# Kernel tuning notes

Hardware: AMD Instinct MI355X
Metric: run time of the kernel (lower is better)

The kernel has to match this reference:

```python
import jax, jax.numpy as jnp
import numpy as np

B, N, F, K = 512, 128, 128, 4


def setup_inputs() -> dict:
    key = jax.random.key(0)
    ks = jax.random.split(key, 12)
    # xavier-normal-ish scales
    s_rw = float(np.sqrt(2.0 / (F + F)))
    s_sw = float(np.sqrt(2.0 / (F + F)))
    inp = {
        "H": jax.random.normal(ks[0], (B, N, F), dtype=jnp.float32),
        "E": jax.random.uniform(ks[1], (B, N, N, K), dtype=jnp.float32),
        "RW1": jax.random.normal(ks[2], (F, F, K), dtype=jnp.float32) * s_rw,
        "SW1": jax.random.normal(ks[3], (F, F), dtype=jnp.float32) * s_sw,
        "RW2": jax.random.normal(ks[4], (F, F, K), dtype=jnp.float32) * s_rw,
        "SW2": jax.random.normal(ks[5], (F, F), dtype=jnp.float32) * s_sw,
        "RW3": jax.random.normal(ks[6], (F, F, K), dtype=jnp.float32) * s_rw,
        "SW3": jax.random.normal(ks[7], (F, F), dtype=jnp.float32) * s_sw,
        "W1": jax.random.normal(ks[8], (F, 20), dtype=jnp.float32) * float(np.sqrt(1.0 / F)),
        "b1": jnp.zeros((20,), dtype=jnp.float32),
        "W2": jax.random.normal(ks[9], (20, 1), dtype=jnp.float32) * float(np.sqrt(1.0 / 20)),
        "b2": jnp.zeros((1,), dtype=jnp.float32),
    }
    return inp


def _rgcn_conv(H, E, D, RW, SW):
    # einsum('bi,bijk,bjm,mnk->bin') done in two GEMM-shaped steps
    M = jnp.einsum('bijk,bjm->bimk', E, H)          # [B,N,F,K]
    msg = jnp.einsum('bimk,mnk->bin', M, RW)        # [B,N,F]
    return jax.nn.sigmoid(msg * D[:, :, None] + jnp.einsum('bij,jl->bil', H, SW))


def reference(H, E, RW1, SW1, RW2, SW2, RW3, SW3, W1, b1, W2, b2):
    # degree norm with self-loops: (E + eye)[b,i,:,:].sum() = E.sum((2,3)) + K
    k = jnp.asarray(E.shape[-1], dtype=E.dtype)
    D = 1.0 / (E.sum(axis=(2, 3)) + k)              # [B,N]
    H = _rgcn_conv(H, E, D, RW1, SW1)
    H = _rgcn_conv(H, E, D, RW2, SW2)
    H = _rgcn_conv(H, E, D, RW3, SW3)
    h = jnp.maximum(H @ W1 + b1, 0.1 * (H @ W1 + b1))  # LeakyReLU(0.1)
    score = jnp.mean(jax.nn.sigmoid(h @ W2 + b2))
    return score
```

## Files before the change

kernel.cpp:

```cpp
#include <hip/hip_runtime.h>
#include <math.h>

#define BB 512
#define NN 128
#define FF 128
#define KK 4
#define GS_PITCH 132

typedef __attribute__((ext_vector_type(8))) short bf16x8;
typedef __attribute__((ext_vector_type(4))) float f32x4;

__device__ inline unsigned short f2bf(float x) {
  union { float f; unsigned int u; } v; v.f = x;
  unsigned int r = v.u + 0x7fff + ((v.u >> 16) & 1);
  return (unsigned short)(r >> 16);
}
__device__ inline float bf2f(unsigned short h) {
  union { unsigned int u; float f; } v; v.u = ((unsigned int)h) << 16; return v.f;
}

__device__ inline void g2l16(const unsigned short* gptr, unsigned short* lptr) {
  __builtin_amdgcn_global_load_lds(
      (const __attribute__((address_space(1))) unsigned int*)gptr,
      (__attribute__((address_space(3))) unsigned int*)lptr, 16, 0, 0);
}

__global__ __launch_bounds__(256) void k_prep(
    const float* __restrict__ E, const float* __restrict__ H,
    const float* __restrict__ RW1, const float* __restrict__ SW1,
    const float* __restrict__ RW2, const float* __restrict__ SW2,
    const float* __restrict__ RW3, const float* __restrict__ SW3,
    unsigned short* __restrict__ Eb, unsigned short* __restrict__ Ha,
    unsigned short* __restrict__ W2L, float* __restrict__ Dv,
    float* __restrict__ Sum, int* __restrict__ Cnt)
{
  const int bid = blockIdx.x;
  if (bid < 16384) {
    int wave = threadIdx.x >> 6;
    int lane = threadIdx.x & 63;
    int row  = bid * 4 + wave;
    const float* p = E + (size_t)row * 512 + lane * 8;
    f32x4 a = *(const f32x4*)p;
    f32x4 b = *(const f32x4*)(p + 4);
    float s = a[0] + a[1] + a[2] + a[3] + b[0] + b[1] + b[2] + b[3];
    #pragma unroll
    for (int off = 32; off > 0; off >>= 1) s += __shfl_down(s, off, 64);
    if (lane == 0) Dv[row] = 1.0f / (s + 4.0f);
    union { unsigned short h[8]; f32x4 v; } u;
    u.h[0] = f2bf(a[0]); u.h[1] = f2bf(a[1]); u.h[2] = f2bf(a[2]); u.h[3] = f2bf(a[3]);
    u.h[4] = f2bf(b[0]); u.h[5] = f2bf(b[1]); u.h[6] = f2bf(b[2]); u.h[7] = f2bf(b[3]);
    *(f32x4*)(Eb + (size_t)row * 512 + lane * 8) = u.v;
  } else if (bid < 20480) {
    size_t i = ((size_t)(bid - 16384) * 256 + threadIdx.x) * 8;
    f32x4 a = *(const f32x4*)(H + i);
    f32x4 b = *(const f32x4*)(H + i + 4);
    union { unsigned short h[8]; f32x4 v; } u;
    u.h[0] = f2bf(a[0]); u.h[1] = f2bf(a[1]); u.h[2] = f2bf(a[2]); u.h[3] = f2bf(a[3]);
    u.h[4] = f2bf(b[0]); u.h[5] = f2bf(b[1]); u.h[6] = f2bf(b[2]); u.h[7] = f2bf(b[3]);
    *(f32x4*)(Ha + i) = u.v;
  } else {
    int t2  = bid - 20480;
    int tab = t2 / 320;
    int idx = (t2 - tab * 320) * 256 + threadIdx.x;
    int m = idx & 127;
    int c = idx >> 7;
    const float* RW = (tab == 0) ? RW1 : (tab == 1) ? RW2 : RW3;
    const float* SW = (tab == 0) ? SW1 : (tab == 1) ? SW2 : SW3;
    float v = (c < 512) ? RW[m * 512 + c] : SW[m * 128 + (c - 512)];
    W2L[(size_t)tab * 81920 + idx] = f2bf(v);
    if (t2 == 0 && threadIdx.x == 0) { *Sum = 0.0f; *Cnt = 0; }
  }
}

template<int DOMLP>
__global__ __launch_bounds__(512, 2) void k_layer(
    const unsigned short* __restrict__ Eb,
    const unsigned short* __restrict__ Hin,
    const unsigned short* __restrict__ W2L,
    const float* __restrict__ Dv,
    unsigned short* __restrict__ Hout,
    const float* __restrict__ W1, const float* __restrict__ b1,
    const float* __restrict__ W2w, const float* __restrict__ b2,
    float* __restrict__ Sum, int* __restrict__ Cnt, float* __restrict__ out)
{
  __shared__ unsigned short Gs[128 * GS_PITCH];
  __shared__ unsigned short Es[128 * 128];

  const int b = blockIdx.x;
  const unsigned short* E_b = Eb  + (size_t)b * 65536;
  const unsigned short* H_b = Hin + (size_t)b * 16384;

  const int tid = threadIdx.x;
  const int w = tid >> 6, l = tid & 63;
  const int wr = w >> 1, wc = w & 1;
  const int lq = l >> 4, lm = l & 15;

  f32x4 macc[2][4] = {};

  for (int s = 0; s < 4; ++s) {
    if (s) __syncthreads();

    bf16x8 fa0[4], fb0[2];
    #pragma unroll
    for (int f = 0; f < 4; ++f)
      fa0[f] = *(const bf16x8*)(W2L + (w * 64 + f * 16 + lm) * 128 + lq * 8);
    #pragma unroll
    for (int g = 0; g < 2; ++g)
      fb0[g] = *(const bf16x8*)(H_b + (s * 32 + g * 16 + lm) * 128 + lq * 8);

    #pragma unroll
    for (int r = 0; r < 4; ++r) {
      int R   = r * 32 + w * 4 + (l >> 4);
      int cbg = (l & 15) ^ (R & 15);
      g2l16(E_b + R * 512 + s * 128 + cbg * 8,
            Es + (r * 32 + w * 4) * 128);
    }

    f32x4 gacc[4][2] = {};
    #pragma unroll
    for (int f = 0; f < 4; ++f)
      #pragma unroll
      for (int g = 0; g < 2; ++g)
        gacc[f][g] = __builtin_amdgcn_mfma_f32_16x16x32_bf16(fa0[f], fb0[g], gacc[f][g], 0, 0, 0);
    #pragma unroll
    for (int k0 = 32; k0 < 128; k0 += 32) {
      bf16x8 fa[4], fb[2];
      #pragma unroll
      for (int f = 0; f < 4; ++f)
        fa[f] = *(const bf16x8*)(W2L + (w * 64 + f * 16 + lm) * 128 + k0 + lq * 8);
      #pragma unroll
      for (int g = 0; g < 2; ++g)
        fb[g] = *(const bf16x8*)(H_b + (s * 32 + g * 16 + lm) * 128 + k0 + lq * 8);
      #pragma unroll
      for (int f = 0; f < 4; ++f)
        #pragma unroll
        for (int g = 0; g < 2; ++g)
          gacc[f][g] = __builtin_amdgcn_mfma_f32_16x16x32_bf16(fa[f], fb[g], gacc[f][g], 0, 0, 0);
    }
    #pragma unroll
    for (int f = 0; f < 4; ++f) {
      int n = w * 16 + f * 4 + lq;
      #pragma unroll
      for (int g = 0; g < 2; ++g) {
        int jl = g * 16 + lm;
        union { unsigned short h4[4]; uint2 v; } u;
        u.h4[0] = f2bf(gacc[f][g][0]); u.h4[1] = f2bf(gacc[f][g][1]);
        u.h4[2] = f2bf(gacc[f][g][2]); u.h4[3] = f2bf(gacc[f][g][3]);
        *(uint2*)(&Gs[n * GS_PITCH + jl * 4]) = u.v;
      }
    }
    __syncthreads();

    #pragma unroll
    for (int kt = 0; kt < 4; ++kt) {
      bf16x8 ea[2], fb[4];
      #pragma unroll
      for (int f = 0; f < 2; ++f) {
        int i  = wr * 32 + f * 16 + lm;
        int cb = (kt * 4 + lq) ^ lm;
        ea[f] = *(const bf16x8*)(Es + i * 128 + cb * 8);
      }
      #pragma unroll
      for (int g = 0; g < 4; ++g)
        fb[g] = *(const bf16x8*)(&Gs[(wc * 64 + g * 16 + lm) * GS_PITCH + kt * 32 + lq * 8]);
      #pragma unroll
      for (int f = 0; f < 2; ++f)
        #pragma unroll
        for (int g = 0; g < 4; ++g)
          macc[f][g] = __builtin_amdgcn_mfma_f32_16x16x32_bf16(ea[f], fb[g], macc[f][g], 0, 0, 0);
    }
  }

  f32x4 sacc[2][4] = {};
  #pragma unroll
  for (int k0 = 0; k0 < 128; k0 += 32) {
    bf16x8 fa[2], fb[4];
    #pragma unroll
    for (int f = 0; f < 2; ++f)
      fa[f] = *(const bf16x8*)(H_b + (wr * 32 + f * 16 + lm) * 128 + k0 + lq * 8);
    #pragma unroll
    for (int g = 0; g < 4; ++g)
      fb[g] = *(const bf16x8*)(W2L + (512 + wc * 64 + g * 16 + lm) * 128 + k0 + lq * 8);
    #pragma unroll
    for (int f = 0; f < 2; ++f)
      #pragma unroll
      for (int g = 0; g < 4; ++g)
        sacc[f][g] = __builtin_amdgcn_mfma_f32_16x16x32_bf16(fa[f], fb[g], sacc[f][g], 0, 0, 0);
  }

  const float* dvb = Dv + b * 128;
  __syncthreads();
  #pragma unroll
  for (int f = 0; f < 2; ++f) {
    int i0 = wr * 32 + f * 16 + lq * 4;
    f32x4 d = *(const f32x4*)(dvb + i0);
    #pragma unroll
    for (int g = 0; g < 4; ++g) {
      int n = wc * 64 + g * 16 + lm;
      #pragma unroll
      for (int r = 0; r < 4; ++r) {
        float v = fmaf(macc[f][g][r], d[r], sacc[f][g][r]);
        Es[(i0 + r) * 128 + n] = f2bf(1.0f / (1.0f + __expf(-v)));
      }
    }
  }
  __syncthreads();
  unsigned short* O_b = Hout + (size_t)b * 16384;
  {
    int off = tid * 32;
    f32x4 v0 = *(const f32x4*)(Es + off);
    f32x4 v1 = *(const f32x4*)(Es + off + 8);
    f32x4 v2 = *(const f32x4*)(Es + off + 16);
    f32x4 v3 = *(const f32x4*)(Es + off + 24);
    *(f32x4*)(O_b + off)      = v0;
    *(f32x4*)(O_b + off + 8)  = v1;
    *(f32x4*)(O_b + off + 16) = v2;
    *(f32x4*)(O_b + off + 24) = v3;
  }

  if (DOMLP) {
    __syncthreads();
    float* W1s = (float*)Gs;
    float* b1s = W1s + 2560;
    float* W2s = b1s + 32;
    float* red = W2s + 32;
    for (int i = tid; i < 2560; i += 512) W1s[i] = W1[i];
    if (tid < 20) { b1s[tid] = b1[tid]; W2s[tid] = W2w[tid]; }
    __syncthreads();

    float sv = 0.0f;
    if (tid < 128) {
      const unsigned short* hr = O_b + (size_t)tid * 128;
      float h[20];
      #pragma unroll
      for (int j = 0; j < 20; ++j) h[j] = b1s[j];
      for (int m8 = 0; m8 < 128; m8 += 8) {
        f32x4 pk = *(const f32x4*)(hr + m8);
        const unsigned short* us = (const unsigned short*)&pk;
        #pragma unroll
        for (int e = 0; e < 8; ++e) {
          float x = bf2f(us[e]);
          #pragma unroll
          for (int j = 0; j < 20; ++j) h[j] = fmaf(x, W1s[(m8 + e) * 20 + j], h[j]);
        }
      }
      float v = b2[0];
      #pragma unroll
      for (int j = 0; j < 20; ++j) {
        float t = h[j];
        t = fmaxf(t, 0.1f * t);
        v = fmaf(t, W2s[j], v);
      }
      sv = 1.0f / (1.0f + __expf(-v));
    }

    red[tid] = sv;
    __syncthreads();
    #pragma unroll
    for (int off = 256; off > 0; off >>= 1) {
      if (tid < off) red[tid] += red[tid + off];
      __syncthreads();
    }
    if (tid == 0) {
      atomicAdd(Sum, red[0]);
      __threadfence();
      int c = atomicAdd(Cnt, 1);
      if (c == BB - 1) {
        float tot = atomicAdd(Sum, 0.0f);
        out[0] = tot * (1.0f / 65536.0f);
      }
    }
  }
}

extern "C" void kernel_launch(void* const* d_in, const int* in_sizes, int n_in,
                              void* d_out, int out_size, void* d_ws, size_t ws_size,
                              hipStream_t stream) {
  (void)in_sizes; (void)n_in; (void)out_size; (void)ws_size;
  const float* H   = (const float*)d_in[0];
  const float* E   = (const float*)d_in[1];
  const float* RW1 = (const float*)d_in[2];
  const float* SW1 = (const float*)d_in[3];
  const float* RW2 = (const float*)d_in[4];
  const float* SW2 = (const float*)d_in[5];
  const float* RW3 = (const float*)d_in[6];
  const float* SW3 = (const float*)d_in[7];
  const float* W1  = (const float*)d_in[8];
  const float* b1  = (const float*)d_in[9];
  const float* W2  = (const float*)d_in[10];
  const float* b2  = (const float*)d_in[11];
  float* out = (float*)d_out;

  char* w = (char*)d_ws;
  float*          wsD   = (float*)w;           w += (size_t)65536 * 4;
  unsigned short* wsEb  = (unsigned short*)w;  w += (size_t)33554432 * 2;
  unsigned short* wsHa  = (unsigned short*)w;  w += (size_t)8388608 * 2;
  unsigned short* wsHb  = (unsigned short*)w;  w += (size_t)8388608 * 2;
  unsigned short* wsHc  = (unsigned short*)w;  w += (size_t)8388608 * 2;
  unsigned short* wsHd  = (unsigned short*)w;  w += (size_t)8388608 * 2;
  unsigned short* wsW2  = (unsigned short*)w;  w += (size_t)3 * 81920 * 2;
  float*          wsSum = (float*)w;           w += 64;
  int*            wsCnt = (int*)w;             w += 64;

  k_prep<<<21440, 256, 0, stream>>>(E, H, RW1, SW1, RW2, SW2, RW3, SW3,
                                    wsEb, wsHa, wsW2, wsD, wsSum, wsCnt);

  k_layer<0><<<BB, 512, 0, stream>>>(wsEb, wsHa, wsW2,          wsD, wsHb,
                                     W1, b1, W2, b2, wsSum, wsCnt, out);
  k_layer<0><<<BB, 512, 0, stream>>>(wsEb, wsHb, wsW2 + 81920,  wsD, wsHc,
                                     W1, b1, W2, b2, wsSum, wsCnt, out);
  k_layer<1><<<BB, 512, 0, stream>>>(wsEb, wsHc, wsW2 + 163840, wsD, wsHd,
                                     W1, b1, W2, b2, wsSum, wsCnt, out);
}
```

Before: 428.0 us.

## Split MLP tail into separate kernel and use raw barriers in layer loop

Moves the final MLP and mean reduction out of the third layer kernel into a dedicated k_mlp kernel that uses one thread per node row across 256 blocks. This stops the third layer kernel from running a mostly idle tail where only 128 of 512 threads work. Inside the layer loop, __syncthreads is replaced with a raw s_barrier, and the barrier before the MFMA phase waits only on LDS counters (lgkmcnt), not on vmcnt. A sched_barrier is added after the async global-to-LDS E loads so the E-tile copy can overlap the first GEMM. The risk is correctness: Es is filled by global_load_lds, which may count against vmcnt, so waiting only on lgkmcnt could let the MFMA phase read Es before the data lands.

```diff
diff --git a/kernel.cpp b/kernel.cpp
--- a/kernel.cpp
+++ b/kernel.cpp
@@ -72,16 +72,12 @@
   }
 }
 
-template<int DOMLP>
 __global__ __launch_bounds__(512, 2) void k_layer(
     const unsigned short* __restrict__ Eb,
     const unsigned short* __restrict__ Hin,
     const unsigned short* __restrict__ W2L,
     const float* __restrict__ Dv,
-    unsigned short* __restrict__ Hout,
-    const float* __restrict__ W1, const float* __restrict__ b1,
-    const float* __restrict__ W2w, const float* __restrict__ b2,
-    float* __restrict__ Sum, int* __restrict__ Cnt, float* __restrict__ out)
+    unsigned short* __restrict__ Hout)
 {
   __shared__ unsigned short Gs[128 * GS_PITCH];
   __shared__ unsigned short Es[128 * 128];
@@ -98,7 +94,7 @@
   f32x4 macc[2][4] = {};
 
   for (int s = 0; s < 4; ++s) {
-    if (s) __syncthreads();
+    if (s) asm volatile("s_barrier" ::: "memory");
 
     bf16x8 fa0[4], fb0[2];
     #pragma unroll
@@ -115,6 +111,7 @@
       g2l16(E_b + R * 512 + s * 128 + cbg * 8,
             Es + (r * 32 + w * 4) * 128);
     }
+    __builtin_amdgcn_sched_barrier(0);
 
     f32x4 gacc[4][2] = {};
     #pragma unroll
@@ -149,7 +146,7 @@
         *(uint2*)(&Gs[n * GS_PITCH + jl * 4]) = u.v;
       }
     }
-    __syncthreads();
+    asm volatile("s_waitcnt lgkmcnt(0)\n\ts_barrier" ::: "memory");
 
     #pragma unroll
     for (int kt = 0; kt < 4; ++kt) {
@@ -217,58 +214,59 @@
     *(f32x4*)(O_b + off + 16) = v2;
     *(f32x4*)(O_b + off + 24) = v3;
   }
-
-  if (DOMLP) {
+}
+
+__global__ __launch_bounds__(256) void k_mlp(
+    const unsigned short* __restrict__ H,
+    const float* __restrict__ W1, const float* __restrict__ b1,
+    const float* __restrict__ W2, const float* __restrict__ b2,
+    float* __restrict__ Sum, int* __restrict__ Cnt, float* __restrict__ out)
+{
+  __shared__ float W1s[128 * 20];
+  __shared__ float b1s[20], W2s[20];
+  __shared__ float red[256];
+  for (int i = threadIdx.x; i < 2560; i += 256) W1s[i] = W1[i];
+  if (threadIdx.x < 20) { b1s[threadIdx.x] = b1[threadIdx.x]; W2s[threadIdx.x] = W2[threadIdx.x]; }
+  __syncthreads();
+
+  int row = blockIdx.x * 256 + threadIdx.x;
+  float h[20];
+  #pragma unroll
+  for (int j = 0; j < 20; ++j) h[j] = b1s[j];
+  const unsigned short* hr = H + (size_t)row * 128;
+  for (int m8 = 0; m8 < 128; m8 += 8) {
+    f32x4 pk = *(const f32x4*)(hr + m8);
+    const unsigned short* us = (const unsigned short*)&pk;
+    #pragma unroll
+    for (int e = 0; e < 8; ++e) {
+      float x = bf2f(us[e]);
+      #pragma unroll
+      for (int j = 0; j < 20; ++j) h[j] = fmaf(x, W1s[(m8 + e) * 20 + j], h[j]);
+    }
+  }
+  float v = b2[0];
+  #pragma unroll
+  for (int j = 0; j < 20; ++j) {
+    float t = h[j];
+    t = fmaxf(t, 0.1f * t);
+    v = fmaf(t, W2s[j], v);
+  }
+  float s = 1.0f / (1.0f + __expf(-v));
+
+  red[threadIdx.x] = s;
+  __syncthreads();
+  #pragma unroll
+  for (int off = 128; off > 0; off >>= 1) {
+    if (threadIdx.x < off) red[threadIdx.x] += red[threadIdx.x + off];
     __syncthreads();
-    float* W1s = (float*)Gs;
-    float* b1s = W1s + 2560;
-    float* W2s = b1s + 32;
-    float* red = W2s + 32;
-    for (int i = tid; i < 2560; i += 512) W1s[i] = W1[i];
-    if (tid < 20) { b1s[tid] = b1[tid]; W2s[tid] = W2w[tid]; }
-    __syncthreads();
-
-    float sv = 0.0f;
-    if (tid < 128) {
-      const unsigned short* hr = O_b + (size_t)tid * 128;
-      float h[20];
-      #pragma unroll
-      for (int j = 0; j < 20; ++j) h[j] = b1s[j];
-      for (int m8 = 0; m8 < 128; m8 += 8) {
-        f32x4 pk = *(const f32x4*)(hr + m8);
-        const unsigned short* us = (const unsigned short*)&pk;
-        #pragma unroll
-        for (int e = 0; e < 8; ++e) {
-          float x = bf2f(us[e]);
-          #pragma unroll
-          for (int j = 0; j < 20; ++j) h[j] = fmaf(x, W1s[(m8 + e) * 20 + j], h[j]);
-        }
-      }
-      float v = b2[0];
-      #pragma unroll
-      for (int j = 0; j < 20; ++j) {
-        float t = h[j];
-        t = fmaxf(t, 0.1f * t);
-        v = fmaf(t, W2s[j], v);
-      }
-      sv = 1.0f / (1.0f + __expf(-v));
-    }
-
-    red[tid] = sv;
-    __syncthreads();
-    #pragma unroll
-    for (int off = 256; off > 0; off >>= 1) {
-      if (tid < off) red[tid] += red[tid + off];
-      __syncthreads();
-    }
-    if (tid == 0) {
-      atomicAdd(Sum, red[0]);
-      __threadfence();
-      int c = atomicAdd(Cnt, 1);
-      if (c == BB - 1) {
-        float tot = atomicAdd(Sum, 0.0f);
-        out[0] = tot * (1.0f / 65536.0f);
-      }
+  }
+  if (threadIdx.x == 0) {
+    atomicAdd(Sum, red[0]);
+    __threadfence();
+    int c = atomicAdd(Cnt, 1);
+    if (c == gridDim.x - 1) {
+      float tot = atomicAdd(Sum, 0.0f);
+      out[0] = tot * (1.0f / 65536.0f);
     }
   }
 }
@@ -305,10 +303,9 @@
   k_prep<<<21440, 256, 0, stream>>>(E, H, RW1, SW1, RW2, SW2, RW3, SW3,
                                     wsEb, wsHa, wsW2, wsD, wsSum, wsCnt);
 
-  k_layer<0><<<BB, 512, 0, stream>>>(wsEb, wsHa, wsW2,          wsD, wsHb,
-                                     W1, b1, W2, b2, wsSum, wsCnt, out);
-  k_layer<0><<<BB, 512, 0, stream>>>(wsEb, wsHb, wsW2 + 81920,  wsD, wsHc,
-                                     W1, b1, W2, b2, wsSum, wsCnt, out);
-  k_layer<1><<<BB, 512, 0, stream>>>(wsEb, wsHc, wsW2 + 163840, wsD, wsHd,
-                                     W1, b1, W2, b2, wsSum, wsCnt, out);
-}
+  k_layer<<<BB, 512, 0, stream>>>(wsEb, wsHa, wsW2,          wsD, wsHb);
+  k_layer<<<BB, 512, 0, stream>>>(wsEb, wsHb, wsW2 + 81920,  wsD, wsHc);
+  k_layer<<<BB, 512, 0, stream>>>(wsEb, wsHc, wsW2 + 163840, wsD, wsHd);
+
+  k_mlp<<<BB * NN / 256, 256, 0, stream>>>(wsHd, W1, b1, W2, b2, wsSum, wsCnt, out);
+}
```

Result: slower. 481.3 us (+12.5%).
